# Kernel tuning notes

Measured on AMD Instinct MI355X. Metric: run time of the kernel, lower is better.

The kernel has to match this reference:

```python
import jax, jax.numpy as jnp
import numpy as np
from jax import lax

LONG_EDGE = 1024
MAX_SIZE = 1333.0
STRIDES = (4, 8, 16, 32, 64)
SIZES = (32, 64, 128, 256, 512)
RATIOS = (0.5, 1.0, 2.0)
PRE_NMS_TOPK = 6000
POST_NMS_TOPK = 1000
NMS_THRESH = 0.7
NUM_CH = 256


def _gen_anchors_level(scale, ratios, shape, stride):
    # faithful copy of generate_anchors_keras (numpy, static)
    scales, ratios = np.meshgrid(np.array([scale], dtype=np.float64), np.array(ratios, dtype=np.float64))
    scales = scales.flatten(); ratios = ratios.flatten()
    size_ratios = stride * stride / ratios
    widths = np.round(np.sqrt(size_ratios))
    heights = np.round(widths * ratios)
    widths = widths * (scales / stride)
    heights = heights * (scales / stride)
    shifts_y = np.arange(0, shape[0]) * stride + (stride - 1) / 2
    shifts_x = np.arange(0, shape[1]) * stride + (stride - 1) / 2
    shifts_x, shifts_y = np.meshgrid(shifts_x, shifts_y)
    box_widths, box_centers_x = np.meshgrid(widths, shifts_x)
    box_heights, box_centers_y = np.meshgrid(heights, shifts_y)
    box_centers = np.stack([box_centers_y, box_centers_x], axis=2).reshape([-1, 2])
    box_sizes = np.stack([box_heights, box_widths], axis=2).reshape([-1, 2])
    boxes = np.concatenate([box_centers - 0.5 * (box_sizes - 1), box_centers + 0.5 * (box_sizes - 1)], axis=1)
    boxes[:, [2, 3]] += 1
    return boxes[:, [1, 0, 3, 2]].astype(np.float32)


def all_anchors():
    shapes = [(int(np.ceil(LONG_EDGE / s)),) * 2 for s in STRIDES]
    return np.concatenate([_gen_anchors_level(SIZES[i], RATIOS, shapes[i], STRIDES[i]) for i in range(len(STRIDES))], axis=0)


def conv2d(x, w, b, padding):
    y = lax.conv_general_dilated(x, w, (1, 1), padding, dimension_numbers=('NCHW', 'OIHW', 'NCHW'))
    return y + b[None, :, None, None]


def decode_bbox_target(deltas, anchors):
    # deltas, anchors: [K,4]
    txty, twth = deltas[:, :2], deltas[:, 2:]
    x1y1, x2y2 = anchors[:, :2], anchors[:, 2:]
    waha = x2y2 - x1y1
    xaya = (x2y2 + x1y1) * 0.5
    clipv = jnp.float32(np.log(MAX_SIZE / 16.0))
    wbhb = jnp.exp(jnp.minimum(twth, clipv)) * waha
    xbyb = txty * waha + xaya
    return jnp.concatenate([xbyb - wbhb * 0.5, xbyb + wbhb * 0.5], axis=1)


def clip_boxes(b, h, w):
    # faithful to source: x clamped to window[0]=h, y to window[1]=w
    return jnp.stack([b[:, 0].clip(0.0, h), b[:, 1].clip(0.0, w), b[:, 2].clip(0.0, h), b[:, 3].clip(0.0, w)], 1)


def nms_keep(boxes, thresh):
    # boxes sorted by descending score; greedy NMS over full IoU matrix
    x1, y1, x2, y2 = boxes[:, 0], boxes[:, 1], boxes[:, 2], boxes[:, 3]
    areas = (x2 - x1) * (y2 - y1)
    iw = jnp.clip(jnp.minimum(x2[:, None], x2[None, :]) - jnp.maximum(x1[:, None], x1[None, :]), 0.0)
    ih = jnp.clip(jnp.minimum(y2[:, None], y2[None, :]) - jnp.maximum(y1[:, None], y1[None, :]), 0.0)
    inter = iw * ih
    iou = inter / (areas[:, None] + areas[None, :] - inter)
    n = boxes.shape[0]
    sup = iou > thresh
    idxs = jnp.arange(n)
    def body(i, keep):
        row = sup[i] & (idxs > i)
        return jnp.where(keep[i], keep & ~row, keep)
    return lax.fori_loop(0, n, body, jnp.ones((n,), bool))


def rpn_forward(image, feats, w0, b0, wcls, bcls, wbox, bbox):
    labels, boxes_l = [], []
    for f in feats:
        hidden = jax.nn.relu(conv2d(f, w0, b0, 'SAME'))
        cls = conv2d(hidden, wcls, bcls, 'VALID')   # [1,A,H,W]
        box = conv2d(hidden, wbox, bbox, 'VALID')   # [1,4A,H,W]
        labels.append(jnp.transpose(cls, (0, 2, 3, 1)).reshape(1, -1, 1))
        boxes_l.append(jnp.transpose(box, (0, 2, 3, 1)).reshape(1, -1, 4))
    scores = jnp.concatenate(labels, axis=1)[0, :, 0]          # [N]
    box_logits = jnp.concatenate(boxes_l, axis=1)[0]           # [N,4]
    anchors = jnp.asarray(all_anchors())                       # [N,4]
    k = min(PRE_NMS_TOPK, anchors.shape[0])
    _, order = lax.top_k(scores, k)
    deltas = box_logits[order]
    pre_anch = anchors[order]
    dec = decode_bbox_target(deltas, pre_anch)
    h, w = float(image.shape[2]), float(image.shape[3])
    boxes = clip_boxes(dec, h, w)
    keep = nms_keep(lax.stop_gradient(boxes), NMS_THRESH)
    sel = jnp.argsort(~keep)[:POST_NMS_TOPK]  # stable: kept boxes in score order, then pad slots
    proposals = jnp.where(keep[sel][:, None], boxes[sel], 0.0)
    return proposals


def setup_inputs() -> dict:
    key = jax.random.key(0)
    ks = jax.random.split(key, 9)
    hw = [256, 128, 64, 32, 16]
    inp = {'image': jax.random.normal(ks[0], (1, 3, 1024, 1024), jnp.float32)}
    for i, s in enumerate(hw):
        inp[f'feat{i}'] = jax.random.normal(jax.random.fold_in(ks[1], i), (1, NUM_CH, s, s), jnp.float32)
    inp['w0'] = jax.random.normal(ks[2], (NUM_CH, NUM_CH, 3, 3), jnp.float32) * 0.01
    inp['b0'] = jnp.zeros((NUM_CH,), jnp.float32)
    inp['wcls'] = jax.random.normal(ks[3], (3, NUM_CH, 1, 1), jnp.float32) * 0.01
    inp['bcls'] = jnp.zeros((3,), jnp.float32)
    inp['wbox'] = jax.random.normal(ks[4], (12, NUM_CH, 1, 1), jnp.float32) * 0.01
    inp['bbox'] = jnp.zeros((12,), jnp.float32)
    return inp


def reference(image, feat0, feat1, feat2, feat3, feat4, w0, b0, wcls, bcls, wbox, bbox):
    feats = [feat0, feat1, feat2, feat3, feat4]
    return rpn_forward(image, feats, w0, b0, wcls, bcls, wbox, bbox)
```

## Files before the change

### kernel.cpp

```cpp
#include <hip/hip_runtime.h>
#include <cstdint>

typedef unsigned long long u64;
typedef unsigned int u32;
typedef unsigned short ushort;
typedef __attribute__((ext_vector_type(8))) short short8;
typedef __attribute__((ext_vector_type(4))) float f32x4;

#define A_TOTAL 261888
#define NPIX    87296
#define KTOP    6000
#define KTARGET 7800
#define NWORDS  94
#define CANDMAX 8192
#define PIXMAX  8192
#define NBINS   16384

__device__ __forceinline__ u64 score_key64(double s) {
  u64 u = (u64)__double_as_longlong(s);
  return (u & 0x8000000000000000ULL) ? ~u : (u | 0x8000000000000000ULL);
}
__device__ __forceinline__ u32 key32(float s) {
  u32 u = __float_as_uint(s);
  return (u & 0x80000000u) ? ~u : (u | 0x80000000u);
}
__device__ __forceinline__ ushort f2bf(float f) {
  u32 u = __float_as_uint(f);
  u32 r = (u + 0x7FFFu + ((u >> 16) & 1u)) >> 16;
  return (ushort)r;
}
__device__ __forceinline__ void pix_level(int pix, int& l, int& off) {
  if (pix < 65536)      { l = 0; off = 0; }
  else if (pix < 81920) { l = 1; off = 65536; }
  else if (pix < 86016) { l = 2; off = 81920; }
  else if (pix < 87040) { l = 3; off = 86016; }
  else                  { l = 4; off = 87040; }
}

__global__ void k_prep_w(const float* __restrict__ w0, double* __restrict__ wt64,
                         ushort* __restrict__ wkf) {
  int i = blockIdx.x * 256 + threadIdx.x;
  if (i < 256 * 2304) {
    int o = i & 255;
    int ictap = i >> 8;
    float v = w0[o * 2304 + ictap];
    wt64[(size_t)ictap * 256 + o] = (double)v;
    int ic = ictap / 9;
    int tap = ictap - ic * 9;
    int w = o >> 6, mt = (o >> 4) & 3, l15 = o & 15;
    int ch = ic >> 5, kk = ic & 31;
    int l4 = kk >> 3, e = kk & 7;
    int lane = l4 * 16 + l15;
    wkf[((((w * 4 + mt) * 8 + ch) * 9 + tap) << 9) + lane * 8 + e] = f2bf(v);
  }
}

__global__ __launch_bounds__(256, 2) void k_conv_mfma(
    const float* __restrict__ f0, const float* __restrict__ f1,
    const float* __restrict__ f2, const float* __restrict__ f3,
    const float* __restrict__ f4,
    const ushort* __restrict__ wkf, const float* __restrict__ b0,
    const float* __restrict__ wcls, const float* __restrict__ bcls,
    float* __restrict__ scr)
{
  __shared__ ushort xsl[100][40];
  __shared__ float  part[3][64][17];

  int b = blockIdx.x;
  int l, tb;
  if (b < 1024)      { l = 0; tb = b; }
  else if (b < 1280) { l = 1; tb = b - 1024; }
  else if (b < 1344) { l = 2; tb = b - 1280; }
  else if (b < 1360) { l = 3; tb = b - 1344; }
  else               { l = 4; tb = b - 1360; }
  const float* feat = (l == 0) ? f0 : (l == 1) ? f1 : (l == 2) ? f2 : (l == 3) ? f3 : f4;
  int Hh = 256 >> l;
  int HW = Hh * Hh;
  int pixOff = (l == 0) ? 0 : (l == 1) ? 65536 : (l == 2) ? 81920 : (l == 3) ? 86016 : 87040;
  int shl = 5 - l;
  int ty = (tb >> shl) << 3;
  int tx = (tb & ((1 << shl) - 1)) << 3;

  int tid = threadIdx.x;
  int w = tid >> 6;
  int lane = tid & 63;
  int l15 = lane & 15;
  int l4 = lane >> 4;

  f32x4 zz = {0.f, 0.f, 0.f, 0.f};
  f32x4 acc[4][4];
  #pragma unroll
  for (int mt = 0; mt < 4; ++mt)
    #pragma unroll
    for (int tt = 0; tt < 4; ++tt) acc[mt][tt] = zz;

  for (int ch = 0; ch < 8; ++ch) {
    __syncthreads();
    for (int e = tid; e < 3200; e += 256) {
      int icl = e / 100;
      int sp = e - icl * 100;
      int yy = sp / 10;
      int xx = sp - yy * 10;
      int gy = ty + yy - 1, gx = tx + xx - 1;
      float v = 0.f;
      if (gy >= 0 && gy < Hh && gx >= 0 && gx < Hh)
        v = feat[(ch * 32 + icl) * HW + gy * Hh + gx];
      xsl[sp][icl] = f2bf(v);
    }
    __syncthreads();
    #pragma unroll
    for (int tap = 0; tap < 9; ++tap) {
      int dy = tap / 3;
      int dx = tap - dy * 3;
      short8 af[4], bf[4];
      #pragma unroll
      for (int mt = 0; mt < 4; ++mt) {
        int abase = ((((w * 4 + mt) * 8 + ch) * 9 + tap) << 9) + (lane << 3);
        af[mt] = *(const short8*)(wkf + abase);
      }
      #pragma unroll
      for (int tt = 0; tt < 4; ++tt) {
        int p = (tt << 4) + l15;
        int sp = ((p >> 3) + dy) * 10 + (p & 7) + dx;
        bf[tt] = *(const short8*)&xsl[sp][l4 << 3];
      }
      #pragma unroll
      for (int mt = 0; mt < 4; ++mt)
        #pragma unroll
        for (int tt = 0; tt < 4; ++tt)
          acc[mt][tt] = __builtin_amdgcn_mfma_f32_16x16x32_bf16(af[mt], bf[tt], acc[mt][tt], 0, 0, 0);
    }
  }

  float pr[3][4];
  #pragma unroll
  for (int kk = 0; kk < 3; ++kk)
    #pragma unroll
    for (int tt = 0; tt < 4; ++tt) pr[kk][tt] = 0.f;
  #pragma unroll
  for (int mt = 0; mt < 4; ++mt) {
    #pragma unroll
    for (int r = 0; r < 4; ++r) {
      int oc = (w << 6) + (mt << 4) + (l4 << 2) + r;
      float bb = b0[oc];
      float c0 = wcls[oc], c1 = wcls[256 + oc], c2 = wcls[512 + oc];
      #pragma unroll
      for (int tt = 0; tt < 4; ++tt) {
        float v = acc[mt][tt][r] + bb;
        v = v > 0.f ? v : 0.f;
        pr[0][tt] = fmaf(c0, v, pr[0][tt]);
        pr[1][tt] = fmaf(c1, v, pr[1][tt]);
        pr[2][tt] = fmaf(c2, v, pr[2][tt]);
      }
    }
  }
  __syncthreads();
  #pragma unroll
  for (int kk = 0; kk < 3; ++kk)
    #pragma unroll
    for (int tt = 0; tt < 4; ++tt)
      part[kk][(tt << 4) + l15][(w << 2) + l4] = pr[kk][tt];
  __syncthreads();
  if (tid < 192) {
    int kk = tid >> 6;
    int px = tid & 63;
    float s = 0.f;
    #pragma unroll
    for (int q = 0; q < 16; ++q) s += part[kk][px][q];
    int pix = pixOff + (ty + (px >> 3)) * Hh + (tx + (px & 7));
    scr[pix * 3 + kk] = s + bcls[kk];
  }
}

__global__ void k_hist1(const float* __restrict__ scr, u32* __restrict__ bins) {
  __shared__ u32 h[NBINS];
  int tid = threadIdx.x;
  for (int idx = tid; idx < NBINS; idx += 256) h[idx] = 0;
  __syncthreads();
  for (int i = blockIdx.x * 256 + tid; i < A_TOTAL; i += gridDim.x * 256)
    atomicAdd(&h[key32(scr[i]) >> 18], 1u);
  __syncthreads();
  for (int idx = tid; idx < NBINS; idx += 256) {
    u32 v = h[idx];
    if (v) atomicAdd(&bins[idx], v);
  }
}

__global__ void k_scan1(const u32* __restrict__ bins, u32* __restrict__ meta) {
  __shared__ u32 psum[256];
  int tid = threadIdx.x;
  u32 s = 0;
  for (int u = 0; u < 64; ++u) s += bins[tid * 64 + u];
  psum[tid] = s;
  __syncthreads();
  if (tid == 0) {
    u32 run = 0;
    for (int t = 255; t >= 0; --t) { u32 tmp = psum[t]; psum[t] = run; run += tmp; }
  }
  __syncthreads();
  u32 cum = psum[tid];
  if (cum < (u32)KTARGET) {
    for (int u = 63; u >= 0; --u) {
      u32 bv = bins[tid * 64 + u];
      u32 nc = cum + bv;
      if (nc >= (u32)KTARGET) {
        meta[0] = (u32)(tid * 64 + u);
        meta[2] = cum;
        break;
      }
      cum = nc;
    }
  }
}

__global__ void k_hist2(const float* __restrict__ scr, const u32* __restrict__ meta,
                        u32* __restrict__ sub) {
  int i = blockIdx.x * 256 + threadIdx.x;
  if (i < A_TOTAL) {
    u32 k = key32(scr[i]);
    if ((k >> 18) == meta[0]) atomicAdd(&sub[(k >> 10) & 0xFFu], 1u);
  }
}

__global__ void k_scan2(const u32* __restrict__ sub, u32* __restrict__ meta) {
  if (threadIdx.x == 0) {
    u32 b = meta[0];
    u32 c = meta[2];
    u32 T = b << 18;
    for (int u = 255; u >= 0; --u) {
      c += sub[u];
      if (c >= (u32)KTARGET) { T = (b << 18) | ((u32)u << 10); break; }
    }
    meta[3] = (T >= (2u << 10)) ? (T - (2u << 10)) : 0u;
  }
}

__global__ void k_cnt2(const float* __restrict__ scr, const u32* __restrict__ meta,
                       u32* __restrict__ blkCnt, u32* __restrict__ blkCntP) {
  __shared__ u32 wc[4], wcp[4];
  int tid = threadIdx.x;
  int lane = tid & 63, wv = tid >> 6;
  u32 T = meta[3];
  int i = blockIdx.x * 256 + tid;
  bool qa = (i < A_TOTAL) && (key32(scr[i]) >= T);
  u64 ba = __ballot(qa);
  bool qp = false;
  if (i < NPIX)
    qp = (key32(scr[i * 3 + 0]) >= T) || (key32(scr[i * 3 + 1]) >= T) || (key32(scr[i * 3 + 2]) >= T);
  u64 bp = __ballot(qp);
  if (lane == 0) { wc[wv] = (u32)__popcll(ba); wcp[wv] = (u32)__popcll(bp); }
  __syncthreads();
  if (tid == 0) {
    blkCnt[blockIdx.x]  = wc[0] + wc[1] + wc[2] + wc[3];
    blkCntP[blockIdx.x] = wcp[0] + wcp[1] + wcp[2] + wcp[3];
  }
}

__global__ __launch_bounds__(1024) void k_scanblk2(const u32* __restrict__ blkCnt,
                                                   u32* __restrict__ blkOff,
                                                   u32* __restrict__ totA,
                                                   const u32* __restrict__ blkCntP,
                                                   u32* __restrict__ blkOffP,
                                                   u32* __restrict__ totP) {
  __shared__ u32 buf[2][1024];
  int tid = threadIdx.x;
  for (int pass = 0; pass < 2; ++pass) {
    const u32* src_ = pass ? blkCntP : blkCnt;
    u32* dst_ = pass ? blkOffP : blkOff;
    u32* tot_ = pass ? totP : totA;
    u32 v = (tid < 1023) ? src_[tid] : 0u;
    buf[0][tid] = v;
    __syncthreads();
    int src = 0;
    for (int d = 1; d < 1024; d <<= 1) {
      u32 t = buf[src][tid] + ((tid >= d) ? buf[src][tid - d] : 0u);
      buf[src ^ 1][tid] = t;
      src ^= 1;
      __syncthreads();
    }
    if (tid < 1023) dst_[tid] = buf[src][tid] - v;
    if (tid == 0) tot_[0] = buf[src][1022];
    __syncthreads();
  }
}

__global__ void k_fill2(const float* __restrict__ scr, const u32* __restrict__ meta,
                        const u32* __restrict__ blkOff, const u32* __restrict__ blkOffP,
                        u32* __restrict__ candIdx, u32* __restrict__ pixList,
                        u32* __restrict__ pixMap) {
  __shared__ u32 wbase[4], wbaseP[4];
  int tid = threadIdx.x;
  int lane = tid & 63, wv = tid >> 6;
  u32 T = meta[3];
  int i = blockIdx.x * 256 + tid;
  bool qa = (i < A_TOTAL) && (key32(scr[i]) >= T);
  u64 ba = __ballot(qa);
  bool qp = false;
  if (i < NPIX)
    qp = (key32(scr[i * 3 + 0]) >= T) || (key32(scr[i * 3 + 1]) >= T) || (key32(scr[i * 3 + 2]) >= T);
  u64 bp = __ballot(qp);
  if (lane == 0) { wbase[wv] = (u32)__popcll(ba); wbaseP[wv] = (u32)__popcll(bp); }
  __syncthreads();
  if (tid == 0) {
    u32 r = blkOff[blockIdx.x];
    #pragma unroll
    for (int w2 = 0; w2 < 4; ++w2) { u32 t = wbase[w2]; wbase[w2] = r; r += t; }
    u32 rp = blkOffP[blockIdx.x];
    #pragma unroll
    for (int w2 = 0; w2 < 4; ++w2) { u32 t = wbaseP[w2]; wbaseP[w2] = rp; rp += t; }
  }
  __syncthreads();
  if (qa) {
    u32 rank = (u32)__popcll(ba & ((1ULL << lane) - 1ULL));
    u32 pos = wbase[wv] + rank;
    if (pos < CANDMAX) candIdx[pos] = (u32)i;
  }
  if (qp) {
    u32 rank = (u32)__popcll(bp & ((1ULL << lane) - 1ULL));
    u32 pos = wbaseP[wv] + rank;
    if (pos < PIXMAX) { pixList[pos] = (u32)i; pixMap[i] = pos; }
  }
}

#define KCH 288
__global__ __launch_bounds__(256, 4) void k_hidden(
    const float* __restrict__ f0, const float* __restrict__ f1,
    const float* __restrict__ f2, const float* __restrict__ f3,
    const float* __restrict__ f4,
    const double* __restrict__ wt64,
    const u32* __restrict__ pixList, const u32* __restrict__ meta,
    double* __restrict__ hpart)
{
  __shared__ float patch[2][KCH][16];
  __shared__ int sValid[16], sY[16], sX[16], sW[16], sL[16];

  int tid = threadIdx.x;
  int pixblk = blockIdx.x >> 1;
  int kc = blockIdx.x & 1;
  int base = pixblk * 16;
  u32 np = meta[4];
  if (np > PIXMAX) np = PIXMAX;
  if (base >= (int)np) return;

  if (tid < 16) {
    int slot = base + tid;
    int v = slot < (int)np;
    sValid[tid] = v;
    int pix = v ? (int)pixList[slot] : 0;
    int l, off;
    pix_level(pix, l, off);
    int W = 256 >> l;
    int idx = pix - off;
    sL[tid] = l;
    sW[tid] = W;
    sY[tid] = idx >> (8 - l);
    sX[tid] = idx & (W - 1);
  }
  __syncthreads();

  auto stage = [&](int cb, int pb) {
    for (int t = tid; t < 1536; t += 256) {
      int s = t & 15;
      int rem = t >> 4;
      int icl = rem / 3;
      int dy = rem - icl * 3;
      int ic = cb * 32 + icl;
      float v0 = 0.f, v1 = 0.f, v2 = 0.f;
      if (sValid[s]) {
        int l = sL[s], W = sW[s], y = sY[s], x = sX[s];
        const float* feat = (l == 0) ? f0 : (l == 1) ? f1 : (l == 2) ? f2 : (l == 3) ? f3 : f4;
        int gy = y + dy - 1;
        if (gy >= 0 && gy < W) {
          const float* rowp = feat + ic * W * W + gy * W;
          if (x - 1 >= 0) v0 = rowp[x - 1];
          v1 = rowp[x];
          if (x + 1 < W) v2 = rowp[x + 1];
        }
      }
      int kb = icl * 9 + dy * 3;
      patch[pb][kb + 0][s] = v0;
      patch[pb][kb + 1][s] = v1;
      patch[pb][kb + 2][s] = v2;
    }
  };

  int ocq = tid & 63;
  int pxq = tid >> 6;

  double acc[4][4];
  #pragma unroll
  for (int i = 0; i < 4; ++i)
    #pragma unroll
    for (int j = 0; j < 4; ++j) acc[i][j] = 0.0;

  int cb0 = kc * 4;
  stage(cb0, 0);
  __syncthreads();

  for (int i = 0; i < 4; ++i) {
    int cb = cb0 + i;
    if (i < 3) stage(cb + 1, (i + 1) & 1);
    const float (*pc)[16] = patch[i & 1];
    const double* wb_ = wt64 + (size_t)(cb * KCH) * 256 + (ocq << 2);
    for (int kk = 0; kk < KCH; ++kk) {
      float4 p4 = *(const float4*)&pc[kk][pxq << 2];
      double pd0 = (double)p4.x, pd1 = (double)p4.y;
      double pd2 = (double)p4.z, pd3 = (double)p4.w;
      const double* wr = wb_ + (size_t)kk * 256;
      double w0_ = wr[0], w1_ = wr[1], w2_ = wr[2], w3_ = wr[3];
      acc[0][0] = fma(w0_, pd0, acc[0][0]);
      acc[0][1] = fma(w0_, pd1, acc[0][1]);
      acc[0][2] = fma(w0_, pd2, acc[0][2]);
      acc[0][3] = fma(w0_, pd3, acc[0][3]);
      acc[1][0] = fma(w1_, pd0, acc[1][0]);
      acc[1][1] = fma(w1_, pd1, acc[1][1]);
      acc[1][2] = fma(w1_, pd2, acc[1][2]);
      acc[1][3] = fma(w1_, pd3, acc[1][3]);
      acc[2][0] = fma(w2_, pd0, acc[2][0]);
      acc[2][1] = fma(w2_, pd1, acc[2][1]);
      acc[2][2] = fma(w2_, pd2, acc[2][2]);
      acc[2][3] = fma(w2_, pd3, acc[2][3]);
      acc[3][0] = fma(w3_, pd0, acc[3][0]);
      acc[3][1] = fma(w3_, pd1, acc[3][1]);
      acc[3][2] = fma(w3_, pd2, acc[3][2]);
      acc[3][3] = fma(w3_, pd3, acc[3][3]);
    }
    __syncthreads();
  }

  #pragma unroll
  for (int j = 0; j < 4; ++j) {
    int s = (pxq << 2) + j;
    if (sValid[s]) {
      double* dst = &hpart[((size_t)kc * PIXMAX + base + s) * 256 + (ocq << 2)];
      dst[0] = acc[0][j];
      dst[1] = acc[1][j];
      dst[2] = acc[2][j];
      dst[3] = acc[3][j];
    }
  }
}

__global__ void k_combine(const double* __restrict__ hpart, const float* __restrict__ b0,
                          const u32* __restrict__ meta, double* __restrict__ hbuf) {
  int b = blockIdx.x;
  u32 np = meta[4];
  if (np > PIXMAX) np = PIXMAX;
  if (b >= (int)np) return;
  int tid = threadIdx.x;
  double p0 = hpart[(size_t)b * 256 + tid];
  double p1 = hpart[((size_t)PIXMAX + b) * 256 + tid];
  double t = (p0 + p1) + (double)b0[tid];
  hbuf[(size_t)b * 256 + tid] = t > 0.0 ? t : 0.0;
}

__global__ __launch_bounds__(256, 4) void k_heads(
    const float* __restrict__ wcls, const float* __restrict__ bcls,
    const float* __restrict__ wbox, const float* __restrict__ bbox,
    const u32* __restrict__ candIdx, const u32* __restrict__ pixMap,
    const u32* __restrict__ meta, const double* __restrict__ hbuf,
    u64* __restrict__ candKey, u32* __restrict__ candPack, double* __restrict__ candDelta)
{
  __shared__ double wavePart[8][5][4];
  __shared__ int sIdx[8], sValid[8], sR[8], sPS[8];
  int tid = threadIdx.x;
  int lane = tid & 63;
  int wv = tid >> 6;
  int base = blockIdx.x * 8;
  u32 cnt = meta[1];
  if (cnt > CANDMAX) cnt = CANDMAX;

  if (base >= (int)cnt) {
    if (tid < 8) {
      candKey[base + tid] = 0ULL;
      candPack[base + tid] = 0xFFFFFFFFu;
    }
    return;
  }

  if (tid < 8) {
    int slot = base + tid;
    int v = slot < (int)cnt;
    sValid[tid] = v;
    int aidx = v ? (int)candIdx[slot] : 0;
    sIdx[tid] = aidx;
    int pix = aidx / 3;
    sR[tid] = aidx - pix * 3;
    sPS[tid] = v ? (int)pixMap[pix] : 0;
  }
  __syncthreads();

  for (int s = 0; s < 8; ++s) {
    if (!sValid[s]) continue;
    int r = sR[s];
    double hv = hbuf[(size_t)sPS[s] * 256 + tid];
    double p0 = (double)wcls[r * 256 + tid] * hv;
    double p1 = (double)wbox[(r * 4 + 0) * 256 + tid] * hv;
    double p2 = (double)wbox[(r * 4 + 1) * 256 + tid] * hv;
    double p3 = (double)wbox[(r * 4 + 2) * 256 + tid] * hv;
    double p4 = (double)wbox[(r * 4 + 3) * 256 + tid] * hv;
    #pragma unroll
    for (int d = 32; d; d >>= 1) {
      p0 += __shfl_xor(p0, d);
      p1 += __shfl_xor(p1, d);
      p2 += __shfl_xor(p2, d);
      p3 += __shfl_xor(p3, d);
      p4 += __shfl_xor(p4, d);
    }
    if (lane == 0) {
      wavePart[s][0][wv] = p0;
      wavePart[s][1][wv] = p1;
      wavePart[s][2][wv] = p2;
      wavePart[s][3][wv] = p3;
      wavePart[s][4][wv] = p4;
    }
  }
  __syncthreads();
  if (tid < 40) {
    int s = tid / 5;
    int k = tid - s * 5;
    int slot = base + s;
    if (sValid[s]) {
      double v = wavePart[s][k][0] + wavePart[s][k][1] + wavePart[s][k][2] + wavePart[s][k][3];
      int r = sR[s];
      if (k == 0) {
        double sc_ = v + (double)bcls[r];
        candKey[slot] = score_key64(sc_);
        candPack[slot] = ((u32)sIdx[s] << 13) | (u32)slot;
      } else {
        candDelta[(size_t)slot * 4 + (k - 1)] = v + (double)bbox[r * 4 + (k - 1)];
      }
    } else if (k == 0) {
      candKey[slot] = 0ULL;
      candPack[slot] = 0xFFFFFFFFu;
    }
  }
}

__global__ __launch_bounds__(256) void k_rank(const u64* __restrict__ candKey,
                                              const u32* __restrict__ candPack,
                                              u32* __restrict__ order) {
  __shared__ u64 fk[1024];
  __shared__ u32 fp[1024];
  __shared__ u32 rsum[32][8];
  int tid = threadIdx.x;
  int c = tid & 31;
  int g = tid >> 5;
  int ci = blockIdx.x * 32 + c;
  u64 mk = candKey[ci];
  u32 mp = candPack[ci];
  u32 cnt = 0;
  for (int chunk = 0; chunk < 8; ++chunk) {
    __syncthreads();
    for (int e = tid; e < 1024; e += 256) {
      fk[e] = candKey[chunk * 1024 + e];
      fp[e] = candPack[chunk * 1024 + e];
    }
    __syncthreads();
    int j0 = g * 128;
    #pragma unroll 4
    for (int j = j0; j < j0 + 128; ++j) {
      u64 kj = fk[j];
      cnt += (kj > mk || (kj == mk && fp[j] < mp)) ? 1u : 0u;
    }
  }
  rsum[c][g] = cnt;
  __syncthreads();
  if (tid < 32) {
    u32 rank = 0;
    #pragma unroll
    for (int q = 0; q < 8; ++q) rank += rsum[tid][q];
    if (rank < (u32)KTOP) order[rank] = mp;
  }
}

__global__ void k_decode(const u32* __restrict__ order, const double* __restrict__ candDelta,
                         double* __restrict__ boxesD) {
  int i = blockIdx.x * 64 + threadIdx.x;
  if (i >= KTOP) return;
  u32 pack = order[i];
  u32 slot = pack & 0x1FFFu;
  u32 a = pack >> 13;
  int pix = (int)(a / 3u);
  int r = (int)(a - (u32)pix * 3u);
  int l, off;
  pix_level(pix, l, off);
  int W = 256 >> l;
  int idx = pix - off;
  int y = idx >> (8 - l);
  int x = idx & (W - 1);
  int s = 4 << l;
  double ratio = (r == 0) ? 0.5 : (r == 1) ? 1.0 : 2.0;
  double wq = rint(sqrt((double)(s * s) / ratio));
  double hq = rint(wq * ratio);
  double Wa = wq * 8.0, Ha = hq * 8.0;
  double cx = (double)x * (double)s + (double)(s - 1) * 0.5;
  double cy = (double)y * (double)s + (double)(s - 1) * 0.5;
  double ax1 = (double)(float)(cx - 0.5 * (Wa - 1.0));
  double ay1 = (double)(float)(cy - 0.5 * (Ha - 1.0));
  double ax2 = (double)(float)(cx + 0.5 * (Wa - 1.0) + 1.0);
  double ay2 = (double)(float)(cy + 0.5 * (Ha - 1.0) + 1.0);
  double tx = candDelta[(size_t)slot * 4 + 0], tyv = candDelta[(size_t)slot * 4 + 1];
  double tw = candDelta[(size_t)slot * 4 + 2], th  = candDelta[(size_t)slot * 4 + 3];
  double wa = ax2 - ax1, ha = ay2 - ay1;
  double xa = (ax1 + ax2) * 0.5, ya = (ay1 + ay2) * 0.5;
  double clipv = (double)(float)log(1333.0 / 16.0);
  double wb = exp(fmin(tw, clipv)) * wa;
  double hb = exp(fmin(th, clipv)) * ha;
  double xb = tx * wa + xa;
  double yb = tyv * ha + ya;
  double bx1 = xb - 0.5 * wb, by1 = yb - 0.5 * hb;
  double bx2 = xb + 0.5 * wb, by2 = yb + 0.5 * hb;
  bx1 = fmin(fmax(bx1, 0.0), 1024.0);
  by1 = fmin(fmax(by1, 0.0), 1024.0);
  bx2 = fmin(fmax(bx2, 0.0), 1024.0);
  by2 = fmin(fmax(by2, 0.0), 1024.0);
  boxesD[(size_t)i * 4 + 0] = bx1;
  boxesD[(size_t)i * 4 + 1] = by1;
  boxesD[(size_t)i * 4 + 2] = bx2;
  boxesD[(size_t)i * 4 + 3] = by2;
}

__global__ void k_mask(const double* __restrict__ boxesD, u64* __restrict__ maskA) {
  __shared__ double cbx[64][4];
  int lane = threadIdx.x;
  int bc = blockIdx.x, br = blockIdx.y;
  if (bc < br) return;
  int ci = bc * 64 + lane;
  if (ci < KTOP) {
    cbx[lane][0] = boxesD[(size_t)ci * 4 + 0];
    cbx[lane][1] = boxesD[(size_t)ci * 4 + 1];
    cbx[lane][2] = boxesD[(size_t)ci * 4 + 2];
    cbx[lane][3] = boxesD[(size_t)ci * 4 + 3];
  } else {
    cbx[lane][0] = -1e30; cbx[lane][1] = -1e30; cbx[lane][2] = -1e30; cbx[lane][3] = -1e30;
  }
  __syncthreads();
  int ri = br * 64 + lane;
  if (ri >= KTOP) return;
  double rx1 = boxesD[(size_t)ri * 4 + 0], ry1 = boxesD[(size_t)ri * 4 + 1];
  double rx2 = boxesD[(size_t)ri * 4 + 2], ry2 = boxesD[(size_t)ri * 4 + 3];
  double ra = (rx2 - rx1) * (ry2 - ry1);
  u64 bits = 0;
  #pragma unroll 4
  for (int j = 0; j < 64; ++j) {
    int cj = bc * 64 + j;
    double iw = fmin(rx2, cbx[j][2]) - fmax(rx1, cbx[j][0]);
    double ih = fmin(ry2, cbx[j][3]) - fmax(ry1, cbx[j][1]);
    iw = fmax(iw, 0.0); ih = fmax(ih, 0.0);
    double inter = iw * ih;
    double ca = (cbx[j][2] - cbx[j][0]) * (cbx[j][3] - cbx[j][1]);
    double iou = inter / (ra + ca - inter);
    if (cj > ri && iou > 0.7) bits |= (1ULL << j);
  }
  maskA[(size_t)ri * NWORDS + bc] = bits;
}

__global__ __launch_bounds__(1024) void k_nms_reduce(const u64* __restrict__ maskA,
                                                     u32* __restrict__ keep) {
  __shared__ u64 rm[NWORDS];
  int tid = threadIdx.x;
  int wv = tid >> 6, lane = tid & 63;
  for (int i = tid; i < NWORDS; i += 1024) rm[i] = 0ULL;
  __syncthreads();
  u64 diagNext = maskA[(size_t)lane * NWORDS + 0];
  int keptTot = 0;
  for (int c = 0; c < NWORDS; ++c) {
    int rows = KTOP - c * 64; if (rows > 64) rows = 64;
    u64 validM = (rows == 64) ? ~0ULL : ((1ULL << rows) - 1ULL);
    size_t rowbase = (size_t)(c * 64 + lane) * NWORDS;
    bool lv = lane < rows;
    int w0i = c + wv;
    u64 v0 = (lv && w0i      < NWORDS) ? maskA[rowbase + w0i]      : 0ULL;
    u64 v1 = (lv && w0i + 16 < NWORDS) ? maskA[rowbase + w0i + 16] : 0ULL;
    u64 v2 = (lv && w0i + 32 < NWORDS) ? maskA[rowbase + w0i + 32] : 0ULL;
    u64 v3 = (lv && w0i + 48 < NWORDS) ? maskA[rowbase + w0i + 48] : 0ULL;
    u64 v4 = (lv && w0i + 64 < NWORDS) ? maskA[rowbase + w0i + 64] : 0ULL;
    u64 v5 = (lv && w0i + 80 < NWORDS) ? maskA[rowbase + w0i + 80] : 0ULL;
    u64 diag = diagNext;
    if (c + 1 < NWORDS) {
      int nrows = KTOP - (c + 1) * 64; if (nrows > 64) nrows = 64;
      diagNext = (lane < nrows) ? maskA[(size_t)((c + 1) * 64 + lane) * NWORDS + (c + 1)] : 0ULL;
    }
    u64 R = rm[c];
    u64 undec = (~R) & validM;
    u64 km = 0;
    while (undec) {
      int j = __builtin_ctzll(undec);
      km |= (1ULL << j);
      u64 dj = (u64)__shfl((unsigned long long)diag, j);
      undec &= ~(dj | (1ULL << j));
    }
    if (wv == 0 && lane < rows) keep[c * 64 + lane] = (u32)((km >> lane) & 1ULL);
    keptTot += (int)__popcll(km);
    if (keptTot >= 1000) {
      for (int i = (c + 1) * 64 + tid; i < KTOP; i += 1024) keep[i] = 0u;
      return;
    }
    u64 sel = ((km >> lane) & 1ULL) ? ~0ULL : 0ULL;
    v0 &= sel; v1 &= sel; v2 &= sel; v3 &= sel; v4 &= sel; v5 &= sel;
    #pragma unroll
    for (int s = 32; s; s >>= 1) {
      v0 |= (u64)__shfl_xor((unsigned long long)v0, s);
      v1 |= (u64)__shfl_xor((unsigned long long)v1, s);
      v2 |= (u64)__shfl_xor((unsigned long long)v2, s);
      v3 |= (u64)__shfl_xor((unsigned long long)v3, s);
      v4 |= (u64)__shfl_xor((unsigned long long)v4, s);
      v5 |= (u64)__shfl_xor((unsigned long long)v5, s);
    }
    if (lane == 0) {
      if (w0i      < NWORDS) rm[w0i]      |= v0;
      if (w0i + 16 < NWORDS) rm[w0i + 16] |= v1;
      if (w0i + 32 < NWORDS) rm[w0i + 32] |= v2;
      if (w0i + 48 < NWORDS) rm[w0i + 48] |= v3;
      if (w0i + 64 < NWORDS) rm[w0i + 64] |= v4;
      if (w0i + 80 < NWORDS) rm[w0i + 80] |= v5;
    }
    __syncthreads();
  }
}

__global__ __launch_bounds__(1024) void k_emit(const u32* __restrict__ keep,
                                               const double* __restrict__ boxesD,
                                               float* __restrict__ out) {
  __shared__ u32 partial[1024];
  __shared__ u32 excl[1024];
  int tid = threadIdx.x;
  for (int j = tid; j < 4000; j += 1024) out[j] = 0.f;
  int base = tid * 6;
  u32 kv[6];
  u32 c = 0;
  #pragma unroll
  for (int u = 0; u < 6; ++u) {
    int j = base + u;
    kv[u] = (j < KTOP) ? keep[j] : 0u;
    c += kv[u];
  }
  partial[tid] = c;
  __syncthreads();
  if (tid == 0) {
    u32 run = 0;
    for (int t = 0; t < 1024; ++t) { excl[t] = run; run += partial[t]; }
  }
  __syncthreads();
  u32 p = excl[tid];
  #pragma unroll
  for (int u = 0; u < 6; ++u) {
    int j = base + u;
    if (j < KTOP && kv[u]) {
      if (p < 1000u) {
        out[p * 4 + 0] = (float)boxesD[(size_t)j * 4 + 0];
        out[p * 4 + 1] = (float)boxesD[(size_t)j * 4 + 1];
        out[p * 4 + 2] = (float)boxesD[(size_t)j * 4 + 2];
        out[p * 4 + 3] = (float)boxesD[(size_t)j * 4 + 3];
      }
      ++p;
    }
  }
}

extern "C" void kernel_launch(void* const* d_in, const int* in_sizes, int n_in,
                              void* d_out, int out_size, void* d_ws, size_t ws_size,
                              hipStream_t stream) {
  const float* f0   = (const float*)d_in[1];
  const float* f1   = (const float*)d_in[2];
  const float* f2   = (const float*)d_in[3];
  const float* f3   = (const float*)d_in[4];
  const float* f4   = (const float*)d_in[5];
  const float* w0   = (const float*)d_in[6];
  const float* b0   = (const float*)d_in[7];
  const float* wcls = (const float*)d_in[8];
  const float* bcls = (const float*)d_in[9];
  const float* wbox = (const float*)d_in[10];
  const float* bbox = (const float*)d_in[11];
  float* out = (float*)d_out;
  char* ws = (char*)d_ws;

  size_t off = 0;
  auto alloc = [&](size_t bytes) { size_t o = off; off += (bytes + 255) & ~(size_t)255; return o; };
  size_t off_scr  = alloc((size_t)A_TOTAL * 4);
  size_t off_w64  = alloc((size_t)256 * 2304 * 8);
  size_t off_wk   = alloc((size_t)256 * 2304 * 2);
  size_t off_hb   = alloc((size_t)PIXMAX * 256 * 8);
  size_t off_hp   = alloc((size_t)2 * PIXMAX * 256 * 8);
  size_t off_ci   = alloc((size_t)CANDMAX * 4);
  size_t off_ck   = alloc((size_t)CANDMAX * 8);
  size_t off_cp   = alloc((size_t)CANDMAX * 4);
  size_t off_cd   = alloc((size_t)CANDMAX * 4 * 8);
  size_t off_pl   = alloc((size_t)PIXMAX * 4);
  size_t off_pm   = alloc((size_t)NPIX * 4);
  size_t off_box  = alloc((size_t)KTOP * 4 * 8);
  size_t off_ord  = alloc((size_t)KTOP * 4);
  size_t off_keep = alloc((size_t)KTOP * 4);
  size_t off_mask = alloc((size_t)KTOP * NWORDS * 8);
  size_t off_bcnt = alloc((size_t)1024 * 4);
  size_t off_boff = alloc((size_t)1024 * 4);
  size_t off_bcp  = alloc((size_t)1024 * 4);
  size_t off_bop  = alloc((size_t)1024 * 4);
  size_t off_bins = alloc((size_t)NBINS * 4);
  size_t off_sub  = alloc((size_t)256 * 4);
  size_t off_meta = alloc((size_t)64 * 4);
  size_t off_end  = off;
  (void)in_sizes; (void)n_in; (void)out_size; (void)ws_size;

  float*  scr       = (float*)(ws + off_scr);
  double* wt64      = (double*)(ws + off_w64);
  ushort* wkf       = (ushort*)(ws + off_wk);
  double* hbuf      = (double*)(ws + off_hb);
  double* hpart     = (double*)(ws + off_hp);
  u32*    candIdx   = (u32*)(ws + off_ci);
  u64*    candKey   = (u64*)(ws + off_ck);
  u32*    candPack  = (u32*)(ws + off_cp);
  double* candDelta = (double*)(ws + off_cd);
  u32*    pixList   = (u32*)(ws + off_pl);
  u32*    pixMap    = (u32*)(ws + off_pm);
  double* boxesD    = (double*)(ws + off_box);
  u32*    order     = (u32*)(ws + off_ord);
  u32*    keep      = (u32*)(ws + off_keep);
  u64*    maskA     = (u64*)(ws + off_mask);
  u32*    blkCnt    = (u32*)(ws + off_bcnt);
  u32*    blkOff    = (u32*)(ws + off_boff);
  u32*    blkCntP   = (u32*)(ws + off_bcp);
  u32*    blkOffP   = (u32*)(ws + off_bop);
  u32*    bins      = (u32*)(ws + off_bins);
  u32*    sub       = (u32*)(ws + off_sub);
  u32*    meta      = (u32*)(ws + off_meta);

  hipMemsetAsync(ws + off_bins, 0, off_end - off_bins, stream);

  k_prep_w<<<2304, 256, 0, stream>>>(w0, wt64, wkf);
  k_conv_mfma<<<1364, 256, 0, stream>>>(f0, f1, f2, f3, f4, wkf, b0, wcls, bcls, scr);
  k_hist1<<<64, 256, 0, stream>>>(scr, bins);
  k_scan1<<<1, 256, 0, stream>>>(bins, meta);
  k_hist2<<<1023, 256, 0, stream>>>(scr, meta, sub);
  k_scan2<<<1, 64, 0, stream>>>(sub, meta);
  k_cnt2<<<1023, 256, 0, stream>>>(scr, meta, blkCnt, blkCntP);
  k_scanblk2<<<1, 1024, 0, stream>>>(blkCnt, blkOff, meta + 1, blkCntP, blkOffP, meta + 4);
  k_fill2<<<1023, 256, 0, stream>>>(scr, meta, blkOff, blkOffP, candIdx, pixList, pixMap);
  k_hidden<<<(PIXMAX / 16) * 2, 256, 0, stream>>>(f0, f1, f2, f3, f4, wt64, pixList, meta, hpart);
  k_combine<<<PIXMAX, 256, 0, stream>>>(hpart, b0, meta, hbuf);
  k_heads<<<CANDMAX / 8, 256, 0, stream>>>(wcls, bcls, wbox, bbox, candIdx, pixMap, meta, hbuf,
                                           candKey, candPack, candDelta);
  k_rank<<<CANDMAX / 32, 256, 0, stream>>>(candKey, candPack, order);
  k_decode<<<94, 64, 0, stream>>>(order, candDelta, boxesD);
  k_mask<<<dim3(NWORDS, NWORDS), 64, 0, stream>>>(boxesD, maskA);
  k_nms_reduce<<<1, 1024, 0, stream>>>(maskA, keep);
  k_emit<<<1, 1024, 0, stream>>>(keep, boxesD, out);
}
```

Measured before the change: 900.0 us.

## Split hidden conv four ways, store weights in fp32, fuse partial-sum combine into heads

The fp64 hidden-layer GEMM is split four ways over input channels instead of two. The channel chunk is halved, and launch bounds are raised so more blocks can be resident. The transposed weights are kept in fp32 and widened to double in registers, which halves weight-load traffic and allows one float4 load per row. The separate combine kernel is removed: k_heads now sums the four partials, adds the bias and applies ReLU inline. The cost is a larger partials buffer and each head block reading four partial vectors per pixel instead of one.

```diff
diff --git a/kernel.cpp b/kernel.cpp
--- a/kernel.cpp
+++ b/kernel.cpp
@@ -37,14 +37,14 @@
   else                  { l = 4; off = 87040; }
 }
 
-__global__ void k_prep_w(const float* __restrict__ w0, double* __restrict__ wt64,
+__global__ void k_prep_w(const float* __restrict__ w0, float* __restrict__ wt32,
                          ushort* __restrict__ wkf) {
   int i = blockIdx.x * 256 + threadIdx.x;
   if (i < 256 * 2304) {
     int o = i & 255;
     int ictap = i >> 8;
     float v = w0[o * 2304 + ictap];
-    wt64[(size_t)ictap * 256 + o] = (double)v;
+    wt32[(size_t)ictap * 256 + o] = v;
     int ic = ictap / 9;
     int tap = ictap - ic * 9;
     int w = o >> 6, mt = (o >> 4) & 3, l15 = o & 15;
@@ -322,12 +322,12 @@
   }
 }
 
-#define KCH 288
-__global__ __launch_bounds__(256, 4) void k_hidden(
+#define KCH 144
+__global__ __launch_bounds__(256, 6) void k_hidden(
     const float* __restrict__ f0, const float* __restrict__ f1,
     const float* __restrict__ f2, const float* __restrict__ f3,
     const float* __restrict__ f4,
-    const double* __restrict__ wt64,
+    const float* __restrict__ wt32,
     const u32* __restrict__ pixList, const u32* __restrict__ meta,
     double* __restrict__ hpart)
 {
@@ -335,8 +335,8 @@
   __shared__ int sValid[16], sY[16], sX[16], sW[16], sL[16];
 
   int tid = threadIdx.x;
-  int pixblk = blockIdx.x >> 1;
-  int kc = blockIdx.x & 1;
+  int pixblk = blockIdx.x >> 2;
+  int kc = blockIdx.x & 3;
   int base = pixblk * 16;
   u32 np = meta[4];
   if (np > PIXMAX) np = PIXMAX;
@@ -359,12 +359,12 @@
   __syncthreads();
 
   auto stage = [&](int cb, int pb) {
-    for (int t = tid; t < 1536; t += 256) {
+    for (int t = tid; t < 768; t += 256) {
       int s = t & 15;
       int rem = t >> 4;
       int icl = rem / 3;
       int dy = rem - icl * 3;
-      int ic = cb * 32 + icl;
+      int ic = cb * 16 + icl;
       float v0 = 0.f, v1 = 0.f, v2 = 0.f;
       if (sValid[s]) {
         int l = sL[s], W = sW[s], y = sY[s], x = sX[s];
@@ -401,13 +401,14 @@
     int cb = cb0 + i;
     if (i < 3) stage(cb + 1, (i + 1) & 1);
     const float (*pc)[16] = patch[i & 1];
-    const double* wb_ = wt64 + (size_t)(cb * KCH) * 256 + (ocq << 2);
+    const float* wb_ = wt32 + (size_t)(cb * KCH) * 256 + (ocq << 2);
     for (int kk = 0; kk < KCH; ++kk) {
       float4 p4 = *(const float4*)&pc[kk][pxq << 2];
       double pd0 = (double)p4.x, pd1 = (double)p4.y;
       double pd2 = (double)p4.z, pd3 = (double)p4.w;
-      const double* wr = wb_ + (size_t)kk * 256;
-      double w0_ = wr[0], w1_ = wr[1], w2_ = wr[2], w3_ = wr[3];
+      float4 wf = *(const float4*)(wb_ + (size_t)kk * 256);
+      double w0_ = (double)wf.x, w1_ = (double)wf.y;
+      double w2_ = (double)wf.z, w3_ = (double)wf.w;
       acc[0][0] = fma(w0_, pd0, acc[0][0]);
       acc[0][1] = fma(w0_, pd1, acc[0][1]);
       acc[0][2] = fma(w0_, pd2, acc[0][2]);
@@ -441,24 +442,12 @@
   }
 }
 
-__global__ void k_combine(const double* __restrict__ hpart, const float* __restrict__ b0,
-                          const u32* __restrict__ meta, double* __restrict__ hbuf) {
-  int b = blockIdx.x;
-  u32 np = meta[4];
-  if (np > PIXMAX) np = PIXMAX;
-  if (b >= (int)np) return;
-  int tid = threadIdx.x;
-  double p0 = hpart[(size_t)b * 256 + tid];
-  double p1 = hpart[((size_t)PIXMAX + b) * 256 + tid];
-  double t = (p0 + p1) + (double)b0[tid];
-  hbuf[(size_t)b * 256 + tid] = t > 0.0 ? t : 0.0;
-}
-
 __global__ __launch_bounds__(256, 4) void k_heads(
     const float* __restrict__ wcls, const float* __restrict__ bcls,
     const float* __restrict__ wbox, const float* __restrict__ bbox,
+    const float* __restrict__ b0,
     const u32* __restrict__ candIdx, const u32* __restrict__ pixMap,
-    const u32* __restrict__ meta, const double* __restrict__ hbuf,
+    const u32* __restrict__ meta, const double* __restrict__ hpart,
     u64* __restrict__ candKey, u32* __restrict__ candPack, double* __restrict__ candDelta)
 {
   __shared__ double wavePart[8][5][4];
@@ -490,10 +479,17 @@
   }
   __syncthreads();
 
+  double bb = (double)b0[tid];
   for (int s = 0; s < 8; ++s) {
     if (!sValid[s]) continue;
     int r = sR[s];
-    double hv = hbuf[(size_t)sPS[s] * 256 + tid];
+    size_t ps = (size_t)sPS[s];
+    double hv = hpart[ps * 256 + tid];
+    hv = hv + hpart[((size_t)PIXMAX + ps) * 256 + tid];
+    hv = hv + hpart[((size_t)2 * PIXMAX + ps) * 256 + tid];
+    hv = hv + hpart[((size_t)3 * PIXMAX + ps) * 256 + tid];
+    hv = hv + bb;
+    hv = hv > 0.0 ? hv : 0.0;
     double p0 = (double)wcls[r * 256 + tid] * hv;
     double p1 = (double)wbox[(r * 4 + 0) * 256 + tid] * hv;
     double p2 = (double)wbox[(r * 4 + 1) * 256 + tid] * hv;
@@ -779,10 +775,9 @@
   size_t off = 0;
   auto alloc = [&](size_t bytes) { size_t o = off; off += (bytes + 255) & ~(size_t)255; return o; };
   size_t off_scr  = alloc((size_t)A_TOTAL * 4);
-  size_t off_w64  = alloc((size_t)256 * 2304 * 8);
+  size_t off_wt   = alloc((size_t)256 * 2304 * 4);
   size_t off_wk   = alloc((size_t)256 * 2304 * 2);
-  size_t off_hb   = alloc((size_t)PIXMAX * 256 * 8);
-  size_t off_hp   = alloc((size_t)2 * PIXMAX * 256 * 8);
+  size_t off_hp   = alloc((size_t)4 * PIXMAX * 256 * 8);
   size_t off_ci   = alloc((size_t)CANDMAX * 4);
   size_t off_ck   = alloc((size_t)CANDMAX * 8);
   size_t off_cp   = alloc((size_t)CANDMAX * 4);
@@ -804,9 +799,8 @@
   (void)in_sizes; (void)n_in; (void)out_size; (void)ws_size;
 
   float*  scr       = (float*)(ws + off_scr);
-  double* wt64      = (double*)(ws + off_w64);
+  float*  wt32      = (float*)(ws + off_wt);
   ushort* wkf       = (ushort*)(ws + off_wk);
-  double* hbuf      = (double*)(ws + off_hb);
   double* hpart     = (double*)(ws + off_hp);
   u32*    candIdx   = (u32*)(ws + off_ci);
   u64*    candKey   = (u64*)(ws + off_ck);
@@ -828,7 +822,7 @@
 
   hipMemsetAsync(ws + off_bins, 0, off_end - off_bins, stream);
 
-  k_prep_w<<<2304, 256, 0, stream>>>(w0, wt64, wkf);
+  k_prep_w<<<2304, 256, 0, stream>>>(w0, wt32, wkf);
   k_conv_mfma<<<1364, 256, 0, stream>>>(f0, f1, f2, f3, f4, wkf, b0, wcls, bcls, scr);
   k_hist1<<<64, 256, 0, stream>>>(scr, bins);
   k_scan1<<<1, 256, 0, stream>>>(bins, meta);
@@ -837,10 +831,9 @@
   k_cnt2<<<1023, 256, 0, stream>>>(scr, meta, blkCnt, blkCntP);
   k_scanblk2<<<1, 1024, 0, stream>>>(blkCnt, blkOff, meta + 1, blkCntP, blkOffP, meta + 4);
   k_fill2<<<1023, 256, 0, stream>>>(scr, meta, blkOff, blkOffP, candIdx, pixList, pixMap);
-  k_hidden<<<(PIXMAX / 16) * 2, 256, 0, stream>>>(f0, f1, f2, f3, f4, wt64, pixList, meta, hpart);
-  k_combine<<<PIXMAX, 256, 0, stream>>>(hpart, b0, meta, hbuf);
-  k_heads<<<CANDMAX / 8, 256, 0, stream>>>(wcls, bcls, wbox, bbox, candIdx, pixMap, meta, hbuf,
-                                           candKey, candPack, candDelta);
+  k_hidden<<<(PIXMAX / 16) * 4, 256, 0, stream>>>(f0, f1, f2, f3, f4, wt32, pixList, meta, hpart);
+  k_heads<<<CANDMAX / 8, 256, 0, stream>>>(wcls, bcls, wbox, bbox, b0, candIdx, pixMap, meta,
+                                           hpart, candKey, candPack, candDelta);
   k_rank<<<CANDMAX / 32, 256, 0, stream>>>(candKey, candPack, order);
   k_decode<<<94, 64, 0, stream>>>(order, candDelta, boxesD);
   k_mask<<<dim3(NWORDS, NWORDS), 64, 0, stream>>>(boxesD, maskA);
```

New measurement: 928.8 us. 3.2% more time.
